# Performance work log

Hardware: AMD Instinct MI355X
Metric: run time of the kernel (lower is better)

## Reference

```python
import jax, jax.numpy as jnp
import numpy as np

LN_EPS = 1e-5  # nn.LayerNorm default
N_HEAD = 12


def layer_norm(x, w, b, eps=LN_EPS):
    m = jnp.mean(x, axis=-1, keepdims=True)
    v = jnp.var(x, axis=-1, keepdims=True)
    return (x - m) * jax.lax.rsqrt(v + eps) * w + b


def mha(x, in_proj_w, in_proj_b, out_w, out_b, n_head):
    # x: [B,S,D]; self-attention, q=k=v=x (torch nn.MultiheadAttention math)
    B, S, D = x.shape
    hd = D // n_head
    qkv = x @ in_proj_w.T + in_proj_b              # [B,S,3D]
    q, k, v = jnp.split(qkv, 3, axis=-1)
    q = q.reshape(B, S, n_head, hd)
    k = k.reshape(B, S, n_head, hd)
    v = v.reshape(B, S, n_head, hd)
    scale = 1.0 / jnp.sqrt(jnp.asarray(hd, x.dtype))
    scores = jnp.einsum('bqhd,bkhd->bhqk', q, k) * scale  # [B,H,S,S]
    attn = jax.nn.softmax(scores, axis=-1)
    o = jnp.einsum('bhqk,bkhd->bqhd', attn, v).reshape(B, S, D)
    return o @ out_w.T + out_b


def setup_inputs() -> dict:
    key = jax.random.key(0)
    ks = jax.random.split(key, 8)
    B, S, D = 4, 2048, 768
    d_ff = 4 * D
    sd = 0.02
    return {
        'x': jax.random.normal(ks[0], (B, S, D), jnp.float32),
        'ln1_w': jnp.ones((D,), jnp.float32),
        'ln1_b': jnp.zeros((D,), jnp.float32),
        'in_proj_w': jax.random.normal(ks[1], (3 * D, D), jnp.float32) * sd,
        'in_proj_b': jax.random.normal(ks[2], (3 * D,), jnp.float32) * sd,
        'out_w': jax.random.normal(ks[3], (D, D), jnp.float32) * sd,
        'out_b': jax.random.normal(ks[4], (D,), jnp.float32) * sd,
        'ln2_w': jnp.ones((D,), jnp.float32),
        'ln2_b': jnp.zeros((D,), jnp.float32),
        'fc_w': jax.random.normal(ks[5], (d_ff, D), jnp.float32) * sd,
        'fc_b': jnp.zeros((d_ff,), jnp.float32),
        'proj_w': jax.random.normal(ks[6], (D, d_ff), jnp.float32) * sd,
        'proj_b': jnp.zeros((D,), jnp.float32),
    }


def reference(x, ln1_w, ln1_b, in_proj_w, in_proj_b, out_w, out_b,
              ln2_w, ln2_b, fc_w, fc_b, proj_w, proj_b):
    h = layer_norm(x, ln1_w, ln1_b)
    x = x + mha(h, in_proj_w, in_proj_b, out_w, out_b, N_HEAD)
    h2 = layer_norm(x, ln2_w, ln2_b)
    mlp = jax.nn.gelu(h2 @ fc_w.T + fc_b, approximate=False) @ proj_w.T + proj_b
    return x + mlp
```

## Files before the change

### kernel.cpp

```cpp
#include <hip/hip_runtime.h>
#include <hip/hip_bf16.h>
#include <math.h>

#define D_MODEL 768
#define N_HEADS 12
#define HD 64
#define SEQ 2048
#define BATCH 4
#define M_ROWS 8192
#define D_FF 3072
#define QKV_DIM 2304
#define LN_EPS 1e-5f
#define Q_SCALE 0.18033688011112042f

typedef __attribute__((ext_vector_type(8))) short bf16x8;
typedef __attribute__((ext_vector_type(4))) float f32x4;
typedef __hip_bfloat16 bf16;

__device__ __forceinline__ void store_val(float* p, float v) { *p = v; }
__device__ __forceinline__ void store_val(bf16* p, float v) { *p = __float2bfloat16(v); }

__device__ __forceinline__ unsigned int pack_bf16_pair(float a, float b) {
    unsigned int ua = __builtin_bit_cast(unsigned int, a) + 0x8000u;
    unsigned int ub = __builtin_bit_cast(unsigned int, b) + 0x8000u;
    return __builtin_amdgcn_perm(ub, ua, 0x07060302u);
}

__device__ __forceinline__ void async_load16(const void* g, void* l) {
    __builtin_amdgcn_global_load_lds(
        (const __attribute__((address_space(1))) void*)g,
        (__attribute__((address_space(3))) void*)l, 16, 0, 0);
}

__global__ __launch_bounds__(256) void ln1_cast(
        const float* __restrict__ x, const float* __restrict__ w,
        const float* __restrict__ b, bf16* __restrict__ y,
        const float* __restrict__ s0, bf16* __restrict__ d0, int n0,
        const float* __restrict__ s1, bf16* __restrict__ d1, int n1,
        const float* __restrict__ s2, bf16* __restrict__ d2, int n2,
        const float* __restrict__ s3, bf16* __restrict__ d3, int n3) {
    int t = threadIdx.x;
    if (blockIdx.x >= M_ROWS) {
        int i = (blockIdx.x - M_ROWS) * 256 + t;
        const float* s; bf16* d; int local = i;
        if (local < n0) { s = s0; d = d0; }
        else {
            local -= n0;
            if (local < n1) { s = s1; d = d1; }
            else {
                local -= n1;
                if (local < n2) { s = s2; d = d2; }
                else {
                    local -= n2;
                    if (local >= n3) return;
                    s = s3; d = d3;
                }
            }
        }
        float4 v = ((const float4*)s)[local];
        uint2 pk;
        pk.x = pack_bf16_pair(v.x, v.y);
        pk.y = pack_bf16_pair(v.z, v.w);
        *(uint2*)(d + local * 4) = pk;
        return;
    }
    int row = blockIdx.x;
    const float* xr = x + (size_t)row * D_MODEL;
    bf16* yr = y + (size_t)row * D_MODEL;
    float v0 = xr[t], v1 = xr[t + 256], v2 = xr[t + 512];
    float s  = v0 + v1 + v2;
    float sq = v0 * v0 + v1 * v1 + v2 * v2;
    #pragma unroll
    for (int off = 32; off; off >>= 1) {
        s  += __shfl_xor(s, off);
        sq += __shfl_xor(sq, off);
    }
    __shared__ float ss[4], ssq[4];
    int wave = t >> 6;
    if ((t & 63) == 0) { ss[wave] = s; ssq[wave] = sq; }
    __syncthreads();
    s  = ss[0] + ss[1] + ss[2] + ss[3];
    sq = ssq[0] + ssq[1] + ssq[2] + ssq[3];
    float mean = s * (1.0f / D_MODEL);
    float var  = sq * (1.0f / D_MODEL) - mean * mean;
    float rstd = rsqrtf(var + LN_EPS);
    yr[t]       = __float2bfloat16((v0 - mean) * rstd * w[t]       + b[t]);
    yr[t + 256] = __float2bfloat16((v1 - mean) * rstd * w[t + 256] + b[t + 256]);
    yr[t + 512] = __float2bfloat16((v2 - mean) * rstd * w[t + 512] + b[t + 512]);
}

template <typename OutT>
__global__ __launch_bounds__(256) void ln_kernel(const float* __restrict__ x,
                                                 const float* __restrict__ w,
                                                 const float* __restrict__ b,
                                                 OutT* __restrict__ y) {
    int row = blockIdx.x;
    const float* xr = x + (size_t)row * D_MODEL;
    OutT* yr = y + (size_t)row * D_MODEL;
    int t = threadIdx.x;
    float v0 = xr[t], v1 = xr[t + 256], v2 = xr[t + 512];
    float s  = v0 + v1 + v2;
    float sq = v0 * v0 + v1 * v1 + v2 * v2;
    #pragma unroll
    for (int off = 32; off; off >>= 1) {
        s  += __shfl_xor(s, off);
        sq += __shfl_xor(sq, off);
    }
    __shared__ float ss[4], ssq[4];
    int wave = t >> 6;
    if ((t & 63) == 0) { ss[wave] = s; ssq[wave] = sq; }
    __syncthreads();
    s  = ss[0] + ss[1] + ss[2] + ss[3];
    sq = ssq[0] + ssq[1] + ssq[2] + ssq[3];
    float mean = s * (1.0f / D_MODEL);
    float var  = sq * (1.0f / D_MODEL) - mean * mean;
    float rstd = rsqrtf(var + LN_EPS);
    store_val(yr + t,       (v0 - mean) * rstd * w[t]       + b[t]);
    store_val(yr + t + 256, (v1 - mean) * rstd * w[t + 256] + b[t + 256]);
    store_val(yr + t + 512, (v2 - mean) * rstd * w[t + 512] + b[t + 512]);
}

__device__ __forceinline__ float gelu_fast(float v) {
    float u = v * (0.7978845608f + 0.0356774081f * v * v);
    u = fminf(fmaxf(u, -10.0f), 10.0f);
    float e = __builtin_amdgcn_exp2f(u * 2.8853900818f);
    float th = (e - 1.0f) * __builtin_amdgcn_rcpf(e + 1.0f);
    return 0.5f * v * (1.0f + th);
}

template <int FUSE, typename OutT, int BM = 128>
__global__ __launch_bounds__(256) void gemm_mfma(const bf16* __restrict__ A,
                                                 const bf16* __restrict__ W,
                                                 const float* __restrict__ bias,
                                                 const float* __restrict__ resid,
                                                 OutT* __restrict__ C,
                                                 int M, int N, int K) {
    const int BK = 64;
    const int LA = BM / 32;
    const int MI = BM / 32;
    __shared__ __align__(16) bf16 As[2][BM * BK];
    __shared__ __align__(16) bf16 Bs[2][128 * BK];
    int t = threadIdx.x;
    int wave = t >> 6, lane = t & 63;

    int nbx = gridDim.x;
    int w0 = blockIdx.x + nbx * blockIdx.y;
    int cpx = (nbx * gridDim.y) >> 3;
    int wg = (w0 & 7) * cpx + (w0 >> 3);
    int m_base = (wg / nbx) * BM, n_base = (wg % nbx) * 128;

    int wm = (wave >> 1) * (BM / 2), wn = (wave & 1) * 64;
    int c = lane & 15, rr = lane >> 4;
    int cx = c & 7;

    f32x4 acc[MI][4] = {};

    const bf16* Ag[LA]; int loffA[LA];
    const bf16* Bg[4];  int loffB[4];
    #pragma unroll
    for (int r = 0; r < LA; r++) {
        int s = r * 256 + t;
        int row = s >> 3, p = s & 7;
        int kc = p ^ (row & 7);
        Ag[r] = A + (size_t)(m_base + row) * K + kc * 8;
        loffA[r] = (r * 256 + wave * 64) * 8;
    }
    #pragma unroll
    for (int r = 0; r < 4; r++) {
        int s = r * 256 + t;
        int row = s >> 3, p = s & 7;
        int kc = p ^ (row & 7);
        Bg[r] = W + (size_t)(n_base + row) * K + kc * 8;
        loffB[r] = (r * 256 + wave * 64) * 8;
    }

    auto STAGE = [&](int kt, int buf) {
        int k0 = kt * BK;
        #pragma unroll
        for (int r = 0; r < LA; r++)
            async_load16(Ag[r] + k0, As[buf] + loffA[r]);
        #pragma unroll
        for (int r = 0; r < 4; r++)
            async_load16(Bg[r] + k0, Bs[buf] + loffB[r]);
    };

    int nk = K / BK;
    STAGE(0, 0);
    STAGE(1, 1);

    for (int ki = 0; ki < nk; ki++) {
        int cur = ki & 1;
        if (ki < nk - 1) {
            if (BM == 128) asm volatile("s_waitcnt vmcnt(8)" ::: "memory");
            else           asm volatile("s_waitcnt vmcnt(6)" ::: "memory");
        } else {
            asm volatile("s_waitcnt vmcnt(0)" ::: "memory");
        }
        __builtin_amdgcn_s_barrier();
        __builtin_amdgcn_sched_barrier(0);

        bf16x8 af[2][MI], bfr[2][4];
        #pragma unroll
        for (int kk = 0; kk < 2; kk++) {
            int sw = ((kk * 4 + rr) ^ cx) * 8;
            #pragma unroll
            for (int mi = 0; mi < MI; mi++)
                af[kk][mi] = *(const bf16x8*)&As[cur][(wm + mi * 16 + c) * BK + sw];
            #pragma unroll
            for (int ni = 0; ni < 4; ni++)
                bfr[kk][ni] = *(const bf16x8*)&Bs[cur][(wn + ni * 16 + c) * BK + sw];
        }
        asm volatile("s_waitcnt lgkmcnt(0)" ::: "memory");
        __builtin_amdgcn_s_barrier();
        __builtin_amdgcn_sched_barrier(0);

        if (ki + 2 < nk) STAGE(ki + 2, cur);

        __builtin_amdgcn_s_setprio(1);
        #pragma unroll
        for (int kk = 0; kk < 2; kk++)
            #pragma unroll
            for (int mi = 0; mi < MI; mi++)
                #pragma unroll
                for (int ni = 0; ni < 4; ni++)
                    acc[mi][ni] = __builtin_amdgcn_mfma_f32_16x16x32_bf16(
                        bfr[kk][ni], af[kk][mi], acc[mi][ni], 0, 0, 0);
        __builtin_amdgcn_s_setprio(0);
    }

    #pragma unroll
    for (int mi = 0; mi < MI; mi++) {
        int m = m_base + wm + mi * 16 + c;
        #pragma unroll
        for (int ni = 0; ni < 4; ni++) {
            int n0 = n_base + wn + ni * 16 + rr * 4;
            float4 bv = *(const float4*)&bias[n0];
            float v0 = acc[mi][ni][0] + bv.x;
            float v1 = acc[mi][ni][1] + bv.y;
            float v2 = acc[mi][ni][2] + bv.z;
            float v3 = acc[mi][ni][3] + bv.w;
            if (FUSE == 1) {
                v0 = gelu_fast(v0); v1 = gelu_fast(v1);
                v2 = gelu_fast(v2); v3 = gelu_fast(v3);
            }
            if (FUSE == 2) {
                float4 rv = *(const float4*)&resid[(size_t)m * N + n0];
                v0 += rv.x; v1 += rv.y; v2 += rv.z; v3 += rv.w;
            }
            if (FUSE == 3 && n0 < 768) {
                v0 *= Q_SCALE; v1 *= Q_SCALE; v2 *= Q_SCALE; v3 *= Q_SCALE;
            }
            OutT* dst = C + (size_t)m * N + n0;
            if (sizeof(OutT) == 4) {
                float4 st = {v0, v1, v2, v3};
                *(float4*)dst = st;
            } else {
                uint2 pk;
                pk.x = pack_bf16_pair(v0, v1);
                pk.y = pack_bf16_pair(v2, v3);
                *(uint2*)dst = pk;
            }
        }
    }
}

__global__ __launch_bounds__(256) void vtrans(const bf16* __restrict__ qkvb,
                                              bf16* __restrict__ vt) {
    __shared__ bf16 T[64 * 72];
    int t = threadIdx.x;
    int s0 = blockIdx.x * 64, h = blockIdx.y, b = blockIdx.z;
    const bf16* src = qkvb + (size_t)(b * SEQ) * QKV_DIM + 2 * D_MODEL + h * HD;
    #pragma unroll
    for (int i = 0; i < 2; i++) {
        int idx = i * 256 + t;
        int sr = idx >> 3, ch = idx & 7;
        uint4 v = *(const uint4*)(src + (size_t)(s0 + sr) * QKV_DIM + ch * 8);
        *(uint4*)&T[sr * 72 + ch * 8] = v;
    }
    __syncthreads();
    int dr = t >> 2, part = t & 3;
    unsigned int w[8];
    #pragma unroll
    for (int i = 0; i < 8; i++) {
        unsigned short a, bsh;
        __builtin_memcpy(&a,   &T[(part * 16 + 2 * i    ) * 72 + dr], 2);
        __builtin_memcpy(&bsh, &T[(part * 16 + 2 * i + 1) * 72 + dr], 2);
        w[i] = (unsigned int)a | ((unsigned int)bsh << 16);
    }
    bf16* dst = vt + ((size_t)((b * N_HEADS + h) * HD + dr)) * SEQ + s0 + part * 16;
    uint4 p0; p0.x = w[0]; p0.y = w[1]; p0.z = w[2]; p0.w = w[3];
    uint4 p1; p1.x = w[4]; p1.y = w[5]; p1.z = w[6]; p1.w = w[7];
    *(uint4*)dst = p0;
    *(uint4*)(dst + 8) = p1;
}

__global__ __launch_bounds__(256) void attn_mfma(const bf16* __restrict__ qkvb,
                                                 const bf16* __restrict__ vt,
                                                 bf16* __restrict__ o) {
    __shared__ __align__(16) bf16 Ks[2 * 64 * 64];
    __shared__ __align__(16) bf16 Vts[2 * 64 * 64];
    __shared__ __align__(16) bf16 Ps[128 * 64];

    int t = threadIdx.x;
    int wave = t >> 6, lane = t & 63;

    int w0 = blockIdx.x + 16 * (blockIdx.y + 12 * blockIdx.z);
    int wg = (w0 & 7) * 96 + (w0 >> 3);
    int qt = wg & 15;
    int hb = wg >> 4;
    int h = hb % 12, b = hb / 12;

    int s0 = qt * 128;
    int wq = wave * 32;
    int c = lane & 15, rr = lane >> 4;
    int cx = c & 7;

    const bf16* qbase  = qkvb + (size_t)b * SEQ * QKV_DIM + h * HD;
    const bf16* kbase  = qbase + D_MODEL;
    const bf16* vtbase = vt + (size_t)((b * N_HEADS + h) * HD) * SEQ;

    #pragma unroll
    for (int r = 0; r < 4; r++) {
        int lin = r * 256 + t;
        int qq = lin >> 3, p = lin & 7;
        int kc = p ^ (qq & 7);
        async_load16(qbase + (size_t)(s0 + qq) * QKV_DIM + kc * 8,
                     Ps + (size_t)(r * 256 + wave * 64) * 8);
    }
    #pragma unroll
    for (int r = 0; r < 2; r++) {
        int row = (r * 256 + t) >> 3;
        int kc = ((r * 256 + t) & 7) ^ (row & 7);
        async_load16(kbase + (size_t)row * QKV_DIM + kc * 8,
                     Ks + (size_t)(r * 256 + wave * 64) * 8);
        async_load16(vtbase + (size_t)row * SEQ + kc * 8,
                     Vts + (size_t)(r * 256 + wave * 64) * 8);
    }
    __syncthreads();

    bf16x8 bq[2][2];
    #pragma unroll
    for (int m = 0; m < 2; m++)
        #pragma unroll
        for (int kk = 0; kk < 2; kk++)
            bq[m][kk] = *(const bf16x8*)&Ps[(wq + m * 16 + c) * 64 + ((kk * 4 + rr) ^ cx) * 8];

    bf16x8 ones;
    #pragma unroll
    for (int i = 0; i < 8; i++) ones[i] = (short)0x3F80;

    f32x4 Oa[2][4] = {};
    f32x4 La[2] = {};

    for (int jt = 0; jt < SEQ; jt += 64) {
        int cur = (jt >> 6) & 1;
        bf16* Kb  = Ks  + cur * 4096;
        bf16* Vtb = Vts + cur * 4096;

        if (jt + 64 < SEQ) {
            bf16* Kn  = Ks  + (cur ^ 1) * 4096;
            bf16* Vtn = Vts + (cur ^ 1) * 4096;
            #pragma unroll
            for (int r = 0; r < 2; r++) {
                int row = (r * 256 + t) >> 3;
                int kc = ((r * 256 + t) & 7) ^ (row & 7);
                async_load16(kbase + (size_t)(jt + 64 + row) * QKV_DIM + kc * 8,
                             Kn + (size_t)(r * 256 + wave * 64) * 8);
                async_load16(vtbase + (size_t)row * SEQ + (jt + 64) + kc * 8,
                             Vtn + (size_t)(r * 256 + wave * 64) * 8);
            }
        }

        f32x4 St[4][2] = {};
        __builtin_amdgcn_s_setprio(1);
        #pragma unroll
        for (int kk = 0; kk < 2; kk++) {
            bf16x8 ak[4];
            #pragma unroll
            for (int jj = 0; jj < 4; jj++)
                ak[jj] = *(const bf16x8*)&Kb[(jj * 16 + c) * 64 + ((kk * 4 + rr) ^ cx) * 8];
            #pragma unroll
            for (int jj = 0; jj < 4; jj++)
                #pragma unroll
                for (int m = 0; m < 2; m++)
                    St[jj][m] = __builtin_amdgcn_mfma_f32_16x16x32_bf16(
                        ak[jj], bq[m][kk], St[jj][m], 0, 0, 0);
        }
        __builtin_amdgcn_s_setprio(0);

        #pragma unroll
        for (int jj = 0; jj < 4; jj++) {
            int off = ((jj * 2 + (rr >> 1)) ^ cx) * 8 + (rr & 1) * 4;
            #pragma unroll
            for (int m = 0; m < 2; m++) {
                float p0 = __builtin_amdgcn_exp2f(St[jj][m][0]);
                float p1 = __builtin_amdgcn_exp2f(St[jj][m][1]);
                float p2 = __builtin_amdgcn_exp2f(St[jj][m][2]);
                float p3 = __builtin_amdgcn_exp2f(St[jj][m][3]);
                uint2 pk;
                pk.x = pack_bf16_pair(p0, p1);
                pk.y = pack_bf16_pair(p2, p3);
                *(uint2*)&Ps[(wq + m * 16 + c) * 64 + off] = pk;
            }
        }

        __builtin_amdgcn_s_setprio(1);
        #pragma unroll
        for (int kk = 0; kk < 2; kk++) {
            bf16x8 ap[2];
            #pragma unroll
            for (int m = 0; m < 2; m++)
                ap[m] = *(const bf16x8*)&Ps[(wq + m * 16 + c) * 64 + ((kk * 4 + rr) ^ cx) * 8];
            #pragma unroll
            for (int m = 0; m < 2; m++)
                La[m] = __builtin_amdgcn_mfma_f32_16x16x32_bf16(
                    ap[m], ones, La[m], 0, 0, 0);
            #pragma unroll
            for (int n = 0; n < 4; n++) {
                bf16x8 bv = *(const bf16x8*)&Vtb[(n * 16 + c) * 64 + ((kk * 4 + rr) ^ cx) * 8];
                #pragma unroll
                for (int m = 0; m < 2; m++)
                    Oa[m][n] = __builtin_amdgcn_mfma_f32_16x16x32_bf16(
                        ap[m], bv, Oa[m][n], 0, 0, 0);
            }
        }
        __builtin_amdgcn_s_setprio(0);

        __syncthreads();
    }

    #pragma unroll
    for (int m = 0; m < 2; m++)
        #pragma unroll
        for (int rg = 0; rg < 4; rg++) {
            float inv = __builtin_amdgcn_rcpf(La[m][rg]);
            int q = s0 + wq + m * 16 + rr * 4 + rg;
            bf16* op = o + (size_t)(b * SEQ + q) * D_MODEL + h * HD;
            #pragma unroll
            for (int n = 0; n < 4; n++)
                op[n * 16 + c] = __float2bfloat16(Oa[m][n][rg] * inv);
        }
}

extern "C" void kernel_launch(void* const* d_in, const int* in_sizes, int n_in,
                              void* d_out, int out_size, void* d_ws, size_t ws_size,
                              hipStream_t stream) {
    const float* x         = (const float*)d_in[0];
    const float* ln1_w     = (const float*)d_in[1];
    const float* ln1_b     = (const float*)d_in[2];
    const float* in_proj_w = (const float*)d_in[3];
    const float* in_proj_b = (const float*)d_in[4];
    const float* out_w     = (const float*)d_in[5];
    const float* out_b     = (const float*)d_in[6];
    const float* ln2_w     = (const float*)d_in[7];
    const float* ln2_b     = (const float*)d_in[8];
    const float* fc_w      = (const float*)d_in[9];
    const float* fc_b      = (const float*)d_in[10];
    const float* proj_w    = (const float*)d_in[11];
    const float* proj_b    = (const float*)d_in[12];

    float* out = (float*)d_out;
    char*  ws  = (char*)d_ws;

    bf16* qkvb = (bf16*)ws;
    bf16* vt   = (bf16*)(ws + 37748736);
    bf16* ff   = (bf16*)ws;
    bf16* h    = (bf16*)(ws + 50331648);
    bf16* o    = (bf16*)(ws + 62914560);
    bf16* wbf  = (bf16*)(ws + 75497472);
    bf16* wqkv_b  = wbf;
    bf16* wout_b  = wqkv_b + (size_t)QKV_DIM * D_MODEL;
    bf16* wfc_b   = wout_b + (size_t)D_MODEL * D_MODEL;
    bf16* wproj_b = wfc_b  + (size_t)D_FF * D_MODEL;

    int n0 = QKV_DIM * D_MODEL / 4, n1 = D_MODEL * D_MODEL / 4;
    int n2 = D_FF * D_MODEL / 4,    n3 = D_MODEL * D_FF / 4;
    int cast_blocks = (n0 + n1 + n2 + n3 + 255) / 256;

    ln1_cast<<<M_ROWS + cast_blocks, 256, 0, stream>>>(
        x, ln1_w, ln1_b, h,
        in_proj_w, wqkv_b, n0, out_w, wout_b, n1, fc_w, wfc_b, n2, proj_w, wproj_b, n3);
    gemm_mfma<3, bf16, 128><<<dim3(QKV_DIM / 128, M_ROWS / 128), 256, 0, stream>>>(
        h, wqkv_b, in_proj_b, nullptr, qkvb, M_ROWS, QKV_DIM, D_MODEL);
    vtrans<<<dim3(SEQ / 64, N_HEADS, BATCH), 256, 0, stream>>>(qkvb, vt);
    attn_mfma<<<dim3(SEQ / 128, N_HEADS, BATCH), 256, 0, stream>>>(qkvb, vt, o);
    gemm_mfma<2, float, 64><<<dim3(D_MODEL / 128, M_ROWS / 64), 256, 0, stream>>>(
        o, wout_b, out_b, x, out, M_ROWS, D_MODEL, D_MODEL);
    ln_kernel<bf16><<<M_ROWS, 256, 0, stream>>>(out, ln2_w, ln2_b, h);
    gemm_mfma<1, bf16, 128><<<dim3(D_FF / 128, M_ROWS / 128), 256, 0, stream>>>(
        h, wfc_b, fc_b, nullptr, ff, M_ROWS, D_FF, D_MODEL);
    gemm_mfma<2, float, 64><<<dim3(D_MODEL / 128, M_ROWS / 64), 256, 0, stream>>>(
        ff, wproj_b, proj_b, out, out, M_ROWS, D_MODEL, D_FF);
}
```

Before: 367.7 us.

## Fuse V transpose into QKV GEMM epilogue and shrink GEMM BM tiles

The QKV projection GEMM now writes the V columns straight into the transposed [b, head*d, seq] layout, so the separate vtrans kernel launch and its round trip through global memory are gone. The QKV and FC GEMMs also switch from BM=128 to BM=64 tiles, which doubles the block count. The transposed stores are scalar 2-byte writes with a stride of SEQ elements, so they coalesce poorly. Smaller tiles give more blocks for occupancy but less operand reuse per block.

After: 364.0 us. Within noise of the previous version (-1.0%).

```diff
diff --git a/kernel.cpp b/kernel.cpp
--- a/kernel.cpp
+++ b/kernel.cpp
@@ -133,6 +133,7 @@
                                                  const bf16* __restrict__ W,
                                                  const float* __restrict__ bias,
                                                  const float* __restrict__ resid,
+                                                 bf16* __restrict__ vtout,
                                                  OutT* __restrict__ C,
                                                  int M, int N, int K) {
     const int BK = 64;
@@ -250,48 +251,28 @@
             if (FUSE == 3 && n0 < 768) {
                 v0 *= Q_SCALE; v1 *= Q_SCALE; v2 *= Q_SCALE; v3 *= Q_SCALE;
             }
-            OutT* dst = C + (size_t)m * N + n0;
-            if (sizeof(OutT) == 4) {
-                float4 st = {v0, v1, v2, v3};
-                *(float4*)dst = st;
+            if (FUSE == 3 && n0 >= 2 * D_MODEL) {
+                int d = n0 - 2 * D_MODEL;
+                int bb = m >> 11, s = m & (SEQ - 1);
+                bf16* vdst = vtout + ((size_t)(bb * D_MODEL + d)) * SEQ + s;
+                vdst[0]        = __float2bfloat16(v0);
+                vdst[SEQ]      = __float2bfloat16(v1);
+                vdst[2 * SEQ]  = __float2bfloat16(v2);
+                vdst[3 * SEQ]  = __float2bfloat16(v3);
             } else {
-                uint2 pk;
-                pk.x = pack_bf16_pair(v0, v1);
-                pk.y = pack_bf16_pair(v2, v3);
-                *(uint2*)dst = pk;
-            }
-        }
-    }
-}
-
-__global__ __launch_bounds__(256) void vtrans(const bf16* __restrict__ qkvb,
-                                              bf16* __restrict__ vt) {
-    __shared__ bf16 T[64 * 72];
-    int t = threadIdx.x;
-    int s0 = blockIdx.x * 64, h = blockIdx.y, b = blockIdx.z;
-    const bf16* src = qkvb + (size_t)(b * SEQ) * QKV_DIM + 2 * D_MODEL + h * HD;
-    #pragma unroll
-    for (int i = 0; i < 2; i++) {
-        int idx = i * 256 + t;
-        int sr = idx >> 3, ch = idx & 7;
-        uint4 v = *(const uint4*)(src + (size_t)(s0 + sr) * QKV_DIM + ch * 8);
-        *(uint4*)&T[sr * 72 + ch * 8] = v;
-    }
-    __syncthreads();
-    int dr = t >> 2, part = t & 3;
-    unsigned int w[8];
-    #pragma unroll
-    for (int i = 0; i < 8; i++) {
-        unsigned short a, bsh;
-        __builtin_memcpy(&a,   &T[(part * 16 + 2 * i    ) * 72 + dr], 2);
-        __builtin_memcpy(&bsh, &T[(part * 16 + 2 * i + 1) * 72 + dr], 2);
-        w[i] = (unsigned int)a | ((unsigned int)bsh << 16);
-    }
-    bf16* dst = vt + ((size_t)((b * N_HEADS + h) * HD + dr)) * SEQ + s0 + part * 16;
-    uint4 p0; p0.x = w[0]; p0.y = w[1]; p0.z = w[2]; p0.w = w[3];
-    uint4 p1; p1.x = w[4]; p1.y = w[5]; p1.z = w[6]; p1.w = w[7];
-    *(uint4*)dst = p0;
-    *(uint4*)(dst + 8) = p1;
+                OutT* dst = C + (size_t)m * N + n0;
+                if (sizeof(OutT) == 4) {
+                    float4 st = {v0, v1, v2, v3};
+                    *(float4*)dst = st;
+                } else {
+                    uint2 pk;
+                    pk.x = pack_bf16_pair(v0, v1);
+                    pk.y = pack_bf16_pair(v2, v3);
+                    *(uint2*)dst = pk;
+                }
+            }
+        }
+    }
 }
 
 __global__ __launch_bounds__(256) void attn_mfma(const bf16* __restrict__ qkvb,
@@ -480,15 +461,14 @@
     ln1_cast<<<M_ROWS + cast_blocks, 256, 0, stream>>>(
         x, ln1_w, ln1_b, h,
         in_proj_w, wqkv_b, n0, out_w, wout_b, n1, fc_w, wfc_b, n2, proj_w, wproj_b, n3);
-    gemm_mfma<3, bf16, 128><<<dim3(QKV_DIM / 128, M_ROWS / 128), 256, 0, stream>>>(
-        h, wqkv_b, in_proj_b, nullptr, qkvb, M_ROWS, QKV_DIM, D_MODEL);
-    vtrans<<<dim3(SEQ / 64, N_HEADS, BATCH), 256, 0, stream>>>(qkvb, vt);
+    gemm_mfma<3, bf16, 64><<<dim3(QKV_DIM / 128, M_ROWS / 64), 256, 0, stream>>>(
+        h, wqkv_b, in_proj_b, nullptr, vt, qkvb, M_ROWS, QKV_DIM, D_MODEL);
     attn_mfma<<<dim3(SEQ / 128, N_HEADS, BATCH), 256, 0, stream>>>(qkvb, vt, o);
     gemm_mfma<2, float, 64><<<dim3(D_MODEL / 128, M_ROWS / 64), 256, 0, stream>>>(
-        o, wout_b, out_b, x, out, M_ROWS, D_MODEL, D_MODEL);
+        o, wout_b, out_b, x, nullptr, out, M_ROWS, D_MODEL, D_MODEL);
     ln_kernel<bf16><<<M_ROWS, 256, 0, stream>>>(out, ln2_w, ln2_b, h);
-    gemm_mfma<1, bf16, 128><<<dim3(D_FF / 128, M_ROWS / 128), 256, 0, stream>>>(
-        h, wfc_b, fc_b, nullptr, ff, M_ROWS, D_FF, D_MODEL);
+    gemm_mfma<1, bf16, 64><<<dim3(D_FF / 128, M_ROWS / 64), 256, 0, stream>>>(
+        h, wfc_b, fc_b, nullptr, nullptr, ff, M_ROWS, D_FF, D_MODEL);
     gemm_mfma<2, float, 64><<<dim3(D_MODEL / 128, M_ROWS / 64), 256, 0, stream>>>(
-        ff, wproj_b, proj_b, out, out, M_ROWS, D_MODEL, D_FF);
-}
+        ff, wproj_b, proj_b, out, nullptr, out, M_ROWS, D_MODEL, D_FF);
+}
```
